# Performance work log

Measured on AMD Instinct MI355X. Metric: run time of the kernel, lower is better.

The kernel has to match this reference:

```python
import jax, jax.numpy as jnp
import numpy as np

B, S, H, NH, FF = 8, 512, 1024, 16, 4096
DK = H // NH


def _ln(x, g, b):
    m = x.mean(-1, keepdims=True)
    v = ((x - m) ** 2).mean(-1, keepdims=True)
    return (x - m) / jnp.sqrt(v + 1e-5) * g + b


def _fwd(x, predicate_pos, attn_bias, attention_mask, atom_graph, variable_graph,
         ln1_g, ln1_b, wq, bq, wk, bk, wv, bv, wo, bo,
         pq_w, pq_b, pk_w, pk_b, pv_w, pv_b, ln2_g, ln2_b, w1, b1, w2, b2):
    b_, s_, h_ = x.shape
    y = _ln(x, ln1_g, ln1_b)
    # ---- self attention (manual MHA with additive bias + mask) ----
    scale = DK ** -0.5
    q = (y @ wq + bq).reshape(b_, s_, NH, DK) * scale
    k = (y @ wk + bk).reshape(b_, s_, NH, DK)
    v = (y @ wv + bv).reshape(b_, s_, NH, DK)
    scores = jnp.einsum('bihd,bjhd->bhij', q, k)
    scores = scores + attn_bias[:, None, :, :] + attention_mask[:, None, :, :]
    att = jax.nn.softmax(scores, axis=-1)
    y_self = jnp.einsum('bhij,bjhd->bihd', att, v).reshape(b_, s_, h_) @ wo + bo
    # ---- path attention (single-head with graph biases) ----
    pscale = h_ ** -0.5
    pq = (y @ pq_w + pq_b) * pscale
    pk = y @ pk_w + pk_b
    pv = y @ pv_w + pv_b
    patt = jnp.einsum('bid,bjd->bij', pq, pk) + atom_graph + variable_graph
    patt = jax.nn.softmax(patt, axis=-1)
    xp = jnp.einsum('bij,bjd->bid', patt, pv)  # [B,S,H]
    # vectorized gather-mean over predicate positions (replaces per-sample loop)
    prev = jnp.concatenate([xp[:, :1], xp[:, :-1]], axis=1)   # xp[i-1]
    nxt = jnp.concatenate([xp[:, 1:], xp[:, -1:]], axis=1)    # xp[i+1]
    a0 = xp[:, 0:2].mean(axis=1, keepdims=True)               # i == 0
    a1 = xp[:, 0:3].mean(axis=1, keepdims=True)               # i == 1
    a2 = (xp + nxt) / 2.0                                     # pos[i-2] == 1
    a3 = (prev + xp + nxt) / 3.0                              # else
    i_arr = jnp.arange(s_)
    pos = (predicate_pos == 1)
    pos_m2 = jnp.pad(pos[:, :-2], ((0, 0), (2, 0)))           # pos[i-2], False for i<2
    atom = jnp.where(pos_m2[..., None], a2, a3)
    atom = jnp.where((i_arr == 1)[None, :, None], a1, atom)
    atom = jnp.where((i_arr == 0)[None, :, None], a0, atom)
    w = pos.astype(xp.dtype)
    path = (atom * w[..., None]).sum(1) / w.sum(1, keepdims=True)  # [B,H]
    y_path = jnp.broadcast_to(path[:, None, :], (b_, s_, h_))
    # ---- combine + residual + FFN ----
    x = x + (y_self + y_path) / 2.0
    y2 = _ln(x, ln2_g, ln2_b)
    hmid = jax.nn.gelu(y2 @ w1 + b1, approximate=False)
    return x + (hmid @ w2 + b2)


def setup_inputs() -> dict:
    key = jax.random.key(0)
    ks = jax.random.split(key, 16)
    def w(k, shape):
        return 0.02 * jax.random.normal(k, shape, dtype=jnp.float32)
    pp = jax.random.randint(ks[0], (B, S), 0, 2, dtype=jnp.int32)
    pp = pp.at[:, 2].set(1).at[:, -1].set(0)  # >=1 predicate; no predicate at last node
    return {
        'x': jax.random.normal(ks[1], (B, S, H), dtype=jnp.float32),
        'predicate_pos': pp,
        'variable_tags': jnp.zeros((B, S), dtype=jnp.int32),
        'attn_bias': 0.1 * jax.random.normal(ks[2], (B, S, S), dtype=jnp.float32),
        'attention_mask': jnp.zeros((B, S, S), dtype=jnp.float32),
        'atom_graph': 0.1 * jax.random.normal(ks[3], (B, S, S), dtype=jnp.float32),
        'variable_graph': 0.1 * jax.random.normal(ks[4], (B, S, S), dtype=jnp.float32),
        'ln1_g': jnp.ones((H,), jnp.float32), 'ln1_b': jnp.zeros((H,), jnp.float32),
        'wq': w(ks[5], (H, H)), 'bq': jnp.zeros((H,), jnp.float32),
        'wk': w(ks[6], (H, H)), 'bk': jnp.zeros((H,), jnp.float32),
        'wv': w(ks[7], (H, H)), 'bv': jnp.zeros((H,), jnp.float32),
        'wo': w(ks[8], (H, H)), 'bo': jnp.zeros((H,), jnp.float32),
        'pq_w': w(ks[9], (H, H)), 'pq_b': jnp.zeros((H,), jnp.float32),
        'pk_w': w(ks[10], (H, H)), 'pk_b': jnp.zeros((H,), jnp.float32),
        'pv_w': w(ks[11], (H, H)), 'pv_b': jnp.zeros((H,), jnp.float32),
        'ln2_g': jnp.ones((H,), jnp.float32), 'ln2_b': jnp.zeros((H,), jnp.float32),
        'w1': w(ks[12], (H, FF)), 'b1': jnp.zeros((FF,), jnp.float32),
        'w2': w(ks[13], (FF, H)), 'b2': jnp.zeros((H,), jnp.float32),
    }


def reference(x, predicate_pos, variable_tags, attn_bias, attention_mask, atom_graph, variable_graph,
              ln1_g, ln1_b, wq, bq, wk, bk, wv, bv, wo, bo,
              pq_w, pq_b, pk_w, pk_b, pv_w, pv_b, ln2_g, ln2_b, w1, b1, w2, b2):
    # variable_tags is unused in the original forward as well
    return _fwd(x, predicate_pos, attn_bias, attention_mask, atom_graph, variable_graph,
                ln1_g, ln1_b, wq, bq, wk, bk, wv, bv, wo, bo,
                pq_w, pq_b, pk_w, pk_b, pv_w, pv_b, ln2_g, ln2_b, w1, b1, w2, b2)
```

## Files before the change

kernel.cpp:

```cpp
#include <hip/hip_runtime.h>
#include <hip/hip_bf16.h>
#include <math.h>


typedef __bf16 bf16x8 __attribute__((ext_vector_type(8)));
typedef float f32x4 __attribute__((ext_vector_type(4)));

__device__ __forceinline__ void async_copy16(void* lds, const void* g) {
  __builtin_amdgcn_global_load_lds(
      (__attribute__((address_space(1))) void*)(void*)g,
      (__attribute__((address_space(3))) void*)lds, 16, 0, 0);
}

__global__ __launch_bounds__(256) void ln_rows_bf16(
    const float* __restrict__ X, const float* __restrict__ G,
    const float* __restrict__ Bt, __hip_bfloat16* __restrict__ O) {
  long row = blockIdx.x;
  int t = threadIdx.x;
  const float4 xv = ((const float4*)(X + row * 1024))[t];
  float s = xv.x + xv.y + xv.z + xv.w;
  float q = xv.x * xv.x + xv.y * xv.y + xv.z * xv.z + xv.w * xv.w;
#pragma unroll
  for (int o = 32; o; o >>= 1) {
    s += __shfl_xor(s, o);
    q += __shfl_xor(q, o);
  }
  __shared__ float rs[4], rq[4];
  int wid = t >> 6;
  if ((t & 63) == 0) { rs[wid] = s; rq[wid] = q; }
  __syncthreads();
  s = rs[0] + rs[1] + rs[2] + rs[3];
  q = rq[0] + rq[1] + rq[2] + rq[3];
  float mean = s * (1.f / 1024.f);
  float var = q * (1.f / 1024.f) - mean * mean;
  float rstd = rsqrtf(var + 1e-5f);
  const float4 gv = ((const float4*)G)[t];
  const float4 bv = ((const float4*)Bt)[t];
  __hip_bfloat16* o = O + row * 1024 + t * 4;
  o[0] = __float2bfloat16((xv.x - mean) * rstd * gv.x + bv.x);
  o[1] = __float2bfloat16((xv.y - mean) * rstd * gv.y + bv.y);
  o[2] = __float2bfloat16((xv.z - mean) * rstd * gv.z + bv.z);
  o[3] = __float2bfloat16((xv.w - mean) * rstd * gv.w + bv.w);
}

struct TC7 {
  const float* in[7];
  __hip_bfloat16* out[7];
  float scale[7];
};
__global__ __launch_bounds__(256) void tconv7(TC7 p) {
  __shared__ float t[32][33];
  int j = blockIdx.z;
  const float* in = p.in[j];
  __hip_bfloat16* out = p.out[j];
  float sc = p.scale[j];
  int c0 = blockIdx.x * 32, r0 = blockIdx.y * 32;
  int tid = threadIdx.x;
  int lr = tid >> 3, lc = (tid & 7) * 4;
  const float4 v = *(const float4*)&in[(long)(r0 + lr) * 1024 + c0 + lc];
  t[lr][lc] = v.x; t[lr][lc + 1] = v.y; t[lr][lc + 2] = v.z; t[lr][lc + 3] = v.w;
  __syncthreads();
  int oc = tid >> 3, orr = (tid & 7) * 4;
  __hip_bfloat16* o = &out[(long)(c0 + oc) * 1024 + r0 + orr];
  o[0] = __float2bfloat16(t[orr][oc] * sc);
  o[1] = __float2bfloat16(t[orr + 1][oc] * sc);
  o[2] = __float2bfloat16(t[orr + 2][oc] * sc);
  o[3] = __float2bfloat16(t[orr + 3][oc] * sc);
}

__global__ __launch_bounds__(256) void tconv_f32_bf16(
    const float* __restrict__ in, __hip_bfloat16* __restrict__ out, int R,
    int C) {
  __shared__ float t[32][33];
  int c0 = blockIdx.x * 32, r0 = blockIdx.y * 32;
  int tid = threadIdx.x;
  int lr = tid >> 3, lc = (tid & 7) * 4;
  const float4 v = *(const float4*)&in[(long)(r0 + lr) * C + c0 + lc];
  t[lr][lc] = v.x; t[lr][lc + 1] = v.y; t[lr][lc + 2] = v.z; t[lr][lc + 3] = v.w;
  __syncthreads();
  int oc = tid >> 3, orr = (tid & 7) * 4;
  __hip_bfloat16* o = &out[(long)(c0 + oc) * R + r0 + orr];
  o[0] = __float2bfloat16(t[orr][oc]);
  o[1] = __float2bfloat16(t[orr + 1][oc]);
  o[2] = __float2bfloat16(t[orr + 2][oc]);
  o[3] = __float2bfloat16(t[orr + 3][oc]);
}

__global__ __launch_bounds__(256) void tconv_bf16(
    const __hip_bfloat16* __restrict__ in, __hip_bfloat16* __restrict__ out,
    int R, int C, int ldin, long sIn) {
  __shared__ __hip_bfloat16 t[32][34];
  int bz = blockIdx.z;
  long ibase = (long)bz * sIn;
  long obase = (long)bz * R * C;
  int c0 = blockIdx.x * 32, r0 = blockIdx.y * 32;
  int tid = threadIdx.x;
  int lr = tid >> 3, lc = (tid & 7) * 4;
  const __hip_bfloat16* ip = &in[ibase + (long)(r0 + lr) * ldin + c0 + lc];
  t[lr][lc] = ip[0]; t[lr][lc + 1] = ip[1]; t[lr][lc + 2] = ip[2]; t[lr][lc + 3] = ip[3];
  __syncthreads();
  int oc = tid >> 3, orr = (tid & 7) * 4;
  __hip_bfloat16* o = &out[obase + (long)(c0 + oc) * R + r0 + orr];
  o[0] = t[orr][oc];
  o[1] = t[orr + 1][oc];
  o[2] = t[orr + 2][oc];
  o[3] = t[orr + 3][oc];
}

struct BC6 {
  const float* b[6];
  float scale[6];
};
__global__ __launch_bounds__(256) void bias_concat(BC6 p, float* __restrict__ o) {
  int idx = blockIdx.x * 256 + threadIdx.x;
  int j = idx >> 10, e = idx & 1023;
  o[idx] = p.b[j][e] * p.scale[j];
}

template <int BN>
__global__ __launch_bounds__(512, 2) void gemm256(
    const __hip_bfloat16* __restrict__ A, const __hip_bfloat16* __restrict__ Bt,
    const float* __restrict__ bias, void* __restrict__ C, int K, int lda,
    int ldb, int ldc, int act, int obf) {
  constexpr int NR = BN / 64;
  constexpr int ABYTES = 256 * 128;
  constexpr int BBYTES = BN * 128;
  constexpr int BUF = ABYTES + BBYTES;
  __shared__ char lds[2 * BUF];

  int nwg = gridDim.x * gridDim.y;
  int wg = blockIdx.y * gridDim.x + blockIdx.x;
  int cpx = nwg >> 3;
  int sw = (wg & 7) * cpx + (wg >> 3);
  int bx = sw % gridDim.x, by = sw / gridDim.x;
  const int m0 = by * 256, n0 = bx * BN;

  const int tid = threadIdx.x;
  const int lane = tid & 63, wid = tid >> 6;
  const int wm = wid >> 2, wn = wid & 3;
  const int ll = lane & 15, lh = lane >> 4;

  const char* Ag = (const char*)A;
  const char* Bg = (const char*)Bt;
  const int srow = tid >> 3;
  const int scb = (tid & 7) * 16;

  auto stage = [&](int t, int bsel) {
    char* base = lds + bsel * BUF;
    long kb = (long)t * 128;
#pragma unroll
    for (int l = 0; l < 4; ++l) {
      int row = l * 64 + srow;
      async_copy16(base + row * 128 + scb,
                   Ag + ((long)(m0 + row) * lda) * 2 + kb + scb);
    }
#pragma unroll
    for (int l = 0; l < BN / 64; ++l) {
      int row = l * 64 + srow;
      async_copy16(base + ABYTES + row * 128 + scb,
                   Bg + ((long)(n0 + row) * ldb) * 2 + kb + scb);
    }
  };

  f32x4 acc[8][NR];
#pragma unroll
  for (int m = 0; m < 8; ++m)
#pragma unroll
    for (int n = 0; n < NR; ++n) acc[m][n] = (f32x4){0.f, 0.f, 0.f, 0.f};

  const int nt = K >> 6;
  stage(0, 0);
  asm volatile("s_waitcnt vmcnt(0)" ::: "memory");
  __builtin_amdgcn_s_barrier();

  for (int t = 0; t < nt; ++t) {
    int bt = t & 1;
    if (t + 1 < nt) stage(t + 1, bt ^ 1);
    const char* Ab = lds + bt * BUF;
    const char* Bb = Ab + ABYTES;
#pragma unroll
    for (int ks = 0; ks < 2; ++ks) {
      bf16x8 af[8], bf[NR];
#pragma unroll
      for (int m = 0; m < 8; ++m)
        af[m] = *(const bf16x8*)(Ab + (wm * 128 + m * 16 + ll) * 128 +
                                 ks * 64 + lh * 16);
#pragma unroll
      for (int n = 0; n < NR; ++n)
        bf[n] = *(const bf16x8*)(Bb + (wn * (BN / 4) + n * 16 + ll) * 128 +
                                 ks * 64 + lh * 16);
      __builtin_amdgcn_s_setprio(1);
#pragma unroll
      for (int m = 0; m < 8; ++m)
#pragma unroll
        for (int n = 0; n < NR; ++n)
          acc[m][n] = __builtin_amdgcn_mfma_f32_16x16x32_bf16(af[m], bf[n],
                                                              acc[m][n], 0, 0, 0);
      __builtin_amdgcn_s_setprio(0);
    }
    asm volatile("s_waitcnt vmcnt(0)" ::: "memory");
    __builtin_amdgcn_s_barrier();
  }

#pragma unroll
  for (int m = 0; m < 8; ++m) {
    int row = m0 + wm * 128 + m * 16 + lh * 4;
#pragma unroll
    for (int n = 0; n < NR; ++n) {
      int col = n0 + wn * (BN / 4) + n * 16 + ll;
      float bs = bias ? bias[col] : 0.f;
#pragma unroll
      for (int r = 0; r < 4; ++r) {
        float v = acc[m][n][r] + bs;
        if (act) v = v * 0.5f * (1.f + erff(v * 0.70710678118f));
        long cidx = (long)(row + r) * ldc + col;
        if (obf)
          ((__hip_bfloat16*)C)[cidx] = __float2bfloat16(v);
        else
          ((float*)C)[cidx] = v;
      }
    }
  }
}

__global__ __launch_bounds__(256) void gemm_bf16_nt(
    const __hip_bfloat16* __restrict__ A, const __hip_bfloat16* __restrict__ Bt,
    const float* __restrict__ bias, const float* __restrict__ E1,
    const float* __restrict__ E2, void* __restrict__ C, int K, int lda,
    int ldb, int ldc, long sA, long sB, long sC, long sE, float alpha, int act,
    int obf) {
  __shared__ unsigned short AsU[128 * 32];
  __shared__ unsigned short BsU[128 * 32];
  const int tid = threadIdx.x;
  const int lane = tid & 63, wave = tid >> 6;
  const int wr = wave >> 1, wc = wave & 1;

  int nwg = gridDim.x * gridDim.y;
  int wg = blockIdx.y * gridDim.x + blockIdx.x;
  int bx = blockIdx.x, by = blockIdx.y;
  if ((nwg & 7) == 0) {
    int cpx = nwg >> 3;
    int sw = (wg & 7) * cpx + (wg >> 3);
    bx = sw % gridDim.x;
    by = sw / gridDim.x;
  }
  const int m0 = by * 128, n0 = bx * 128;
  const int bz = blockIdx.z;
  const char* Ab = (const char*)(A + (long)bz * sA);
  const char* Bb = (const char*)(Bt + (long)bz * sB);

  f32x4 acc[4][4];
#pragma unroll
  for (int m = 0; m < 4; ++m)
#pragma unroll
    for (int n = 0; n < 4; ++n) acc[m][n] = (f32x4){0.f, 0.f, 0.f, 0.f};

  const int srow = tid >> 2;
  const int scol = (tid & 3) * 16;
  const int wbase = (tid >> 6) * 1024;

  for (int k0 = 0; k0 < K; k0 += 32) {
#pragma unroll
    for (int i = 0; i < 2; ++i) {
      async_copy16((char*)AsU + i * 4096 + wbase,
                   Ab + ((long)(m0 + i * 64 + srow) * lda + k0) * 2 + scol);
      async_copy16((char*)BsU + i * 4096 + wbase,
                   Bb + ((long)(n0 + i * 64 + srow) * ldb + k0) * 2 + scol);
    }
    __syncthreads();

    const int koff = (lane >> 4) * 8;
    bf16x8 a[4], b[4];
#pragma unroll
    for (int m = 0; m < 4; ++m)
      a[m] = *(const bf16x8*)&AsU[(wr * 64 + m * 16 + (lane & 15)) * 32 + koff];
#pragma unroll
    for (int n = 0; n < 4; ++n)
      b[n] = *(const bf16x8*)&BsU[(wc * 64 + n * 16 + (lane & 15)) * 32 + koff];
#pragma unroll
    for (int m = 0; m < 4; ++m)
#pragma unroll
      for (int n = 0; n < 4; ++n)
        acc[m][n] = __builtin_amdgcn_mfma_f32_16x16x32_bf16(a[m], b[n],
                                                            acc[m][n], 0, 0, 0);
    __syncthreads();
  }

#pragma unroll
  for (int m = 0; m < 4; ++m) {
    int row = m0 + wr * 64 + m * 16 + (lane >> 4) * 4;
#pragma unroll
    for (int n = 0; n < 4; ++n) {
      int col = n0 + wc * 64 + n * 16 + (lane & 15);
      float bs = bias ? bias[col] : 0.f;
#pragma unroll
      for (int r = 0; r < 4; ++r) {
        float v = (acc[m][n][r] + bs) * alpha;
        long eidx = (long)bz * sE + (long)(row + r) * ldc + col;
        if (E1) v += E1[eidx];
        if (E2) v += E2[eidx];
        if (act) v = v * 0.5f * (1.f + erff(v * 0.70710678118f));
        long cidx = (long)bz * sC + (long)(row + r) * ldc + col;
        if (obf)
          ((__hip_bfloat16*)C)[cidx] = __float2bfloat16(v);
        else
          ((float*)C)[cidx] = v;
      }
    }
  }
}

__global__ __launch_bounds__(256) void attn_mfma(
    const __hip_bfloat16* __restrict__ Q, const __hip_bfloat16* __restrict__ K,
    const __hip_bfloat16* __restrict__ VT, const float* __restrict__ BiasP,
    const float* __restrict__ MaskP, __hip_bfloat16* __restrict__ O,
    int ldqk) {
  __shared__ __hip_bfloat16 P[32][520];
  __shared__ float red[2][32][4];
  const int it = blockIdx.x, h = blockIdx.y, b = blockIdx.z;
  const int i0 = it * 32;
  const int tid = threadIdx.x;
  const int lane = tid & 63, w = tid >> 6;
  const int lh = lane >> 4, ll = lane & 15;

  const long qkb = (long)b * 512 * ldqk + h * 64;

  bf16x8 a[2][2];
#pragma unroll
  for (int m = 0; m < 2; ++m)
#pragma unroll
    for (int ks = 0; ks < 2; ++ks)
      a[m][ks] = *(const bf16x8*)&Q[qkb + (long)(i0 + m * 16 + ll) * ldqk +
                                    ks * 32 + lh * 8];

  f32x4 acc[2][8];
#pragma unroll
  for (int m = 0; m < 2; ++m)
#pragma unroll
    for (int n = 0; n < 8; ++n) acc[m][n] = (f32x4){0.f, 0.f, 0.f, 0.f};

#pragma unroll
  for (int n = 0; n < 8; ++n) {
    const __hip_bfloat16* kp =
        &K[qkb + (long)(w * 128 + n * 16 + ll) * ldqk + lh * 8];
    bf16x8 b0 = *(const bf16x8*)&kp[0];
    bf16x8 b1 = *(const bf16x8*)&kp[32];
#pragma unroll
    for (int m = 0; m < 2; ++m) {
      acc[m][n] =
          __builtin_amdgcn_mfma_f32_16x16x32_bf16(a[m][0], b0, acc[m][n], 0, 0, 0);
      acc[m][n] =
          __builtin_amdgcn_mfma_f32_16x16x32_bf16(a[m][1], b1, acc[m][n], 0, 0, 0);
    }
  }

  const long bmo = ((long)b * 512 + i0) * 512 + w * 128;
#pragma unroll
  for (int m = 0; m < 2; ++m)
#pragma unroll
    for (int r = 0; r < 4; ++r) {
      int row = m * 16 + lh * 4 + r;
#pragma unroll
      for (int n = 0; n < 8; ++n) {
        long gi = bmo + (long)row * 512 + n * 16 + ll;
        acc[m][n][r] += BiasP[gi] + MaskP[gi];
      }
    }

  float rmax[2][4];
#pragma unroll
  for (int m = 0; m < 2; ++m)
#pragma unroll
    for (int r = 0; r < 4; ++r) {
      float v = acc[m][0][r];
#pragma unroll
      for (int n = 1; n < 8; ++n) v = fmaxf(v, acc[m][n][r]);
#pragma unroll
      for (int o = 1; o < 16; o <<= 1) v = fmaxf(v, __shfl_xor(v, o));
      rmax[m][r] = v;
    }
  if (ll == 0) {
#pragma unroll
    for (int m = 0; m < 2; ++m)
#pragma unroll
      for (int r = 0; r < 4; ++r) red[0][m * 16 + lh * 4 + r][w] = rmax[m][r];
  }
  __syncthreads();
#pragma unroll
  for (int m = 0; m < 2; ++m)
#pragma unroll
    for (int r = 0; r < 4; ++r) {
      const float* p = red[0][m * 16 + lh * 4 + r];
      rmax[m][r] = fmaxf(fmaxf(p[0], p[1]), fmaxf(p[2], p[3]));
    }
  float rsum[2][4];
#pragma unroll
  for (int m = 0; m < 2; ++m)
#pragma unroll
    for (int r = 0; r < 4; ++r) {
      float s = 0.f;
#pragma unroll
      for (int n = 0; n < 8; ++n) {
        float e = __expf(acc[m][n][r] - rmax[m][r]);
        acc[m][n][r] = e;
        s += e;
      }
#pragma unroll
      for (int o = 1; o < 16; o <<= 1) s += __shfl_xor(s, o);
      rsum[m][r] = s;
    }
  if (ll == 0) {
#pragma unroll
    for (int m = 0; m < 2; ++m)
#pragma unroll
      for (int r = 0; r < 4; ++r) red[1][m * 16 + lh * 4 + r][w] = rsum[m][r];
  }
  __syncthreads();
#pragma unroll
  for (int m = 0; m < 2; ++m)
#pragma unroll
    for (int r = 0; r < 4; ++r) {
      const float* p = red[1][m * 16 + lh * 4 + r];
      float inv = 1.f / (p[0] + p[1] + p[2] + p[3]);
      int row = m * 16 + lh * 4 + r;
#pragma unroll
      for (int n = 0; n < 8; ++n)
        P[row][w * 128 + n * 16 + ll] = __float2bfloat16(acc[m][n][r] * inv);
    }
  __syncthreads();

  const long vtb = ((long)b * 1024 + h * 64) * 512;
  const long ob = (long)b * 512 * 1024 + h * 64;
  const int mw = (w >> 1) * 16, nw = (w & 1) * 32;
  f32x4 oacc[2];
  oacc[0] = (f32x4){0.f, 0.f, 0.f, 0.f};
  oacc[1] = (f32x4){0.f, 0.f, 0.f, 0.f};
#pragma unroll
  for (int ks = 0; ks < 16; ++ks) {
    int k0 = ks * 32;
    bf16x8 pa = *(const bf16x8*)&P[mw + ll][k0 + lh * 8];
#pragma unroll
    for (int nf = 0; nf < 2; ++nf) {
      bf16x8 vb = *(const bf16x8*)&VT[vtb + (long)(nw + nf * 16 + ll) * 512 +
                                      k0 + lh * 8];
      oacc[nf] =
          __builtin_amdgcn_mfma_f32_16x16x32_bf16(pa, vb, oacc[nf], 0, 0, 0);
    }
  }
#pragma unroll
  for (int nf = 0; nf < 2; ++nf)
#pragma unroll
    for (int r = 0; r < 4; ++r)
      O[ob + (long)(i0 + mw + lh * 4 + r) * 1024 + nw + nf * 16 + ll] =
          __float2bfloat16(oacc[nf][r]);
}

__global__ __launch_bounds__(256) void softmax_rows(
    const float* __restrict__ P, __hip_bfloat16* __restrict__ Ob) {
  const float* row = P + (long)blockIdx.x * 512;
  __hip_bfloat16* orow = Ob + (long)blockIdx.x * 512;
  int t = threadIdx.x;
  float v0 = row[t], v1 = row[t + 256];
  float m = fmaxf(v0, v1);
#pragma unroll
  for (int o = 32; o; o >>= 1) m = fmaxf(m, __shfl_xor(m, o));
  __shared__ float red[8];
  int wid = t >> 6, lane = t & 63;
  if (!lane) red[wid] = m;
  __syncthreads();
  m = fmaxf(fmaxf(red[0], red[1]), fmaxf(red[2], red[3]));
  float e0 = __expf(v0 - m), e1 = __expf(v1 - m);
  float s = e0 + e1;
#pragma unroll
  for (int o = 32; o; o >>= 1) s += __shfl_xor(s, o);
  if (!lane) red[4 + wid] = s;
  __syncthreads();
  s = red[4] + red[5] + red[6] + red[7];
  float inv = 1.f / s;
  orow[t] = __float2bfloat16(e0 * inv);
  orow[t + 256] = __float2bfloat16(e1 * inv);
}

__global__ __launch_bounds__(256) void path_partial(
    const float* __restrict__ xp, const int* __restrict__ pp,
    float* __restrict__ PP, float* __restrict__ WS) {
  int b = blockIdx.x, hc = blockIdx.y, ic = blockIdx.z;
  int h = hc * 256 + threadIdx.x;
  const int* ppb = pp + b * 512;
  const float* xb = xp + (long)b * 512 * 1024;
  int iA = ic * 64, iB = iA + 64;
  float acc = 0.f;
  for (int i = iA; i < iB; ++i) {
    if (ppb[i] != 1) continue;
    float cur = xb[(long)i * 1024 + h];
    float a;
    if (i == 0) {
      a = 0.5f * (cur + xb[1024 + h]);
    } else if (i == 1) {
      a = (xb[h] + cur + xb[2 * 1024 + h]) * (1.f / 3.f);
    } else {
      int inx = (i + 1 < 512) ? i + 1 : 511;
      float nx = xb[(long)inx * 1024 + h];
      if (ppb[i - 2] == 1) {
        a = 0.5f * (cur + nx);
      } else {
        a = (xb[(long)(i - 1) * 1024 + h] + cur + nx) * (1.f / 3.f);
      }
    }
    acc += a;
  }
  PP[((long)b * 8 + ic) * 1024 + h] = acc;
  if (hc == 0 && threadIdx.x == 0) {
    float c = 0.f;
    for (int i = iA; i < iB; ++i) c += (ppb[i] == 1) ? 1.f : 0.f;
    WS[b * 8 + ic] = c;
  }
}

__global__ __launch_bounds__(256) void path_finalize(
    const float* __restrict__ PP, const float* __restrict__ WS,
    float* __restrict__ PATH) {
  int b = blockIdx.x;
  int h = blockIdx.y * 256 + threadIdx.x;
  float s = 0.f, w = 0.f;
#pragma unroll
  for (int ic = 0; ic < 8; ++ic) {
    s += PP[((long)b * 8 + ic) * 1024 + h];
    w += WS[b * 8 + ic];
  }
  PATH[b * 1024 + h] = s / w;
}

__global__ __launch_bounds__(256) void combine_ln2(
    const float* __restrict__ X, const float* __restrict__ YS,
    const float* __restrict__ PT, const float* __restrict__ G,
    const float* __restrict__ Bt, float* __restrict__ X2,
    __hip_bfloat16* __restrict__ Y2b) {
  long row = blockIdx.x;
  int b = (int)(row >> 9);
  int t = threadIdx.x;
  const float4 xv = ((const float4*)(X + row * 1024))[t];
  const float4 sv = ((const float4*)(YS + row * 1024))[t];
  const float4 pv = *(const float4*)(PT + b * 1024 + t * 4);
  float4 v;
  v.x = xv.x + 0.5f * (sv.x + pv.x);
  v.y = xv.y + 0.5f * (sv.y + pv.y);
  v.z = xv.z + 0.5f * (sv.z + pv.z);
  v.w = xv.w + 0.5f * (sv.w + pv.w);
  ((float4*)(X2 + row * 1024))[t] = v;

  float s = v.x + v.y + v.z + v.w;
  float q = v.x * v.x + v.y * v.y + v.z * v.z + v.w * v.w;
#pragma unroll
  for (int o = 32; o; o >>= 1) {
    s += __shfl_xor(s, o);
    q += __shfl_xor(q, o);
  }
  __shared__ float rs[4], rq[4];
  int wid = t >> 6;
  if ((t & 63) == 0) { rs[wid] = s; rq[wid] = q; }
  __syncthreads();
  s = rs[0] + rs[1] + rs[2] + rs[3];
  q = rq[0] + rq[1] + rq[2] + rq[3];
  float mean = s * (1.f / 1024.f);
  float var = q * (1.f / 1024.f) - mean * mean;
  float rstd = rsqrtf(var + 1e-5f);
  const float4 gv = ((const float4*)G)[t];
  const float4 bv = ((const float4*)Bt)[t];
  __hip_bfloat16* o = Y2b + row * 1024 + t * 4;
  o[0] = __float2bfloat16((v.x - mean) * rstd * gv.x + bv.x);
  o[1] = __float2bfloat16((v.y - mean) * rstd * gv.y + bv.y);
  o[2] = __float2bfloat16((v.z - mean) * rstd * gv.z + bv.z);
  o[3] = __float2bfloat16((v.w - mean) * rstd * gv.w + bv.w);
}

extern "C" void kernel_launch(void* const* d_in, const int* in_sizes, int n_in,
                              void* d_out, int out_size, void* d_ws,
                              size_t ws_size, hipStream_t stream) {
  const float* x = (const float*)d_in[0];
  const int* pp = (const int*)d_in[1];
  const float* abias = (const float*)d_in[3];
  const float* amask = (const float*)d_in[4];
  const float* agraph = (const float*)d_in[5];
  const float* vgraph = (const float*)d_in[6];
  const float* ln1g = (const float*)d_in[7];
  const float* ln1b = (const float*)d_in[8];
  const float* wq = (const float*)d_in[9];
  const float* bq = (const float*)d_in[10];
  const float* wk = (const float*)d_in[11];
  const float* bk = (const float*)d_in[12];
  const float* wv = (const float*)d_in[13];
  const float* bv = (const float*)d_in[14];
  const float* wo = (const float*)d_in[15];
  const float* bo = (const float*)d_in[16];
  const float* pqw = (const float*)d_in[17];
  const float* pqb = (const float*)d_in[18];
  const float* pkw = (const float*)d_in[19];
  const float* pkb = (const float*)d_in[20];
  const float* pvw = (const float*)d_in[21];
  const float* pvb = (const float*)d_in[22];
  const float* ln2g = (const float*)d_in[23];
  const float* ln2b = (const float*)d_in[24];
  const float* w1 = (const float*)d_in[25];
  const float* b1 = (const float*)d_in[26];
  const float* w2 = (const float*)d_in[27];
  const float* b2 = (const float*)d_in[28];

  char* wsb = (char*)d_ws;
  auto Ybf = (__hip_bfloat16*)(wsb);
  auto QKV = (__hip_bfloat16*)(wsb + (8l << 20));
  auto VTb = (__hip_bfloat16*)(wsb + (56l << 20));
  auto PVT = (__hip_bfloat16*)(wsb + (64l << 20));
  auto ATTb = (__hip_bfloat16*)(wsb + (72l << 20));
  auto PATTb = (__hip_bfloat16*)(wsb + (88l << 20));
  auto PATTf = (float*)(wsb + (92l << 20));
  auto XP = (float*)(wsb + (92l << 20));
  auto WALL = (__hip_bfloat16*)(wsb + (108l << 20));
  auto WOT = (__hip_bfloat16*)(wsb + (120l << 20));
  auto W1T = (__hip_bfloat16*)(wsb + (122l << 20));
  auto bias6 = (float*)(wsb + (130l << 20));
  auto PPart = (float*)(wsb + (131l << 20));
  auto WSp = (float*)(wsb + (132l << 20));
  auto PATH = (float*)(wsb + (133l << 20));
  auto YSELF = (float*)(wsb + (8l << 20));
  auto X2 = (float*)(wsb + (24l << 20));
  auto HMID = (__hip_bfloat16*)(wsb + (40l << 20));
  auto W2T = ATTb;
  __hip_bfloat16* Y2b = Ybf;
  float* OUT = (float*)d_out;

  const float qscale = 0.125f;
  const float pscale = 0.03125f;
  const long S2 = 512l * 512;
  const long SQ = 512l * 6144;

  __hip_bfloat16* Qp = QKV;
  __hip_bfloat16* Kp = QKV + 1024;
  __hip_bfloat16* Vp = QKV + 2048;
  __hip_bfloat16* PQp = QKV + 3072;
  __hip_bfloat16* PKp = QKV + 4096;
  __hip_bfloat16* PVp = QKV + 5120;

  TC7 tp;
  tp.in[0] = wq;  tp.out[0] = WALL;                 tp.scale[0] = qscale;
  tp.in[1] = wk;  tp.out[1] = WALL + 1024 * 1024;   tp.scale[1] = 1.f;
  tp.in[2] = wv;  tp.out[2] = WALL + 2048 * 1024;   tp.scale[2] = 1.f;
  tp.in[3] = pqw; tp.out[3] = WALL + 3072 * 1024;   tp.scale[3] = pscale;
  tp.in[4] = pkw; tp.out[4] = WALL + 4096 * 1024;   tp.scale[4] = 1.f;
  tp.in[5] = pvw; tp.out[5] = WALL + 5120 * 1024;   tp.scale[5] = 1.f;
  tp.in[6] = wo;  tp.out[6] = WOT;                  tp.scale[6] = 1.f;
  tconv7<<<dim3(32, 32, 7), 256, 0, stream>>>(tp);
  tconv_f32_bf16<<<dim3(128, 32), 256, 0, stream>>>(w1, W1T, 1024, 4096);

  BC6 bp;
  bp.b[0] = bq;  bp.scale[0] = qscale;
  bp.b[1] = bk;  bp.scale[1] = 1.f;
  bp.b[2] = bv;  bp.scale[2] = 1.f;
  bp.b[3] = pqb; bp.scale[3] = pscale;
  bp.b[4] = pkb; bp.scale[4] = 1.f;
  bp.b[5] = pvb; bp.scale[5] = 1.f;
  bias_concat<<<24, 256, 0, stream>>>(bp, bias6);

  ln_rows_bf16<<<4096, 256, 0, stream>>>(x, ln1g, ln1b, Ybf);

  gemm256<128><<<dim3(48, 16), 512, 0, stream>>>(
      Ybf, WALL, bias6, QKV, 1024, 1024, 1024, 6144, 0, 1);

  tconv_bf16<<<dim3(32, 16, 8), 256, 0, stream>>>(Vp, VTb, 512, 1024, 6144, SQ);
  tconv_bf16<<<dim3(32, 16, 8), 256, 0, stream>>>(PVp, PVT, 512, 1024, 6144, SQ);

  gemm_bf16_nt<<<dim3(4, 4, 8), 256, 0, stream>>>(
      PQp, PKp, nullptr, agraph, vgraph, PATTf, 1024, 6144, 6144, 512, SQ, SQ,
      S2, S2, 1.f, 0, 0);
  softmax_rows<<<4096, 256, 0, stream>>>(PATTf, PATTb);

  attn_mfma<<<dim3(16, 16, 8), 256, 0, stream>>>(Qp, Kp, VTb, abias, amask,
                                                 ATTb, 6144);

  gemm_bf16_nt<<<dim3(8, 4, 8), 256, 0, stream>>>(
      PATTb, PVT, nullptr, nullptr, nullptr, XP, 512, 512, 512, 1024, S2,
      512l * 1024, 512l * 1024, 0, 1.f, 0, 0);

  path_partial<<<dim3(8, 4, 8), 256, 0, stream>>>(XP, pp, PPart, WSp);
  path_finalize<<<dim3(8, 4), 256, 0, stream>>>(PPart, WSp, PATH);

  gemm_bf16_nt<<<dim3(8, 32, 1), 256, 0, stream>>>(
      ATTb, WOT, bo, nullptr, nullptr, YSELF, 1024, 1024, 1024, 1024, 0, 0, 0,
      0, 1.f, 0, 0);

  tconv_f32_bf16<<<dim3(32, 128), 256, 0, stream>>>(w2, W2T, 4096, 1024);

  combine_ln2<<<4096, 256, 0, stream>>>(x, YSELF, PATH, ln2g, ln2b, X2, Y2b);

  gemm256<256><<<dim3(16, 16), 512, 0, stream>>>(
      Y2b, W1T, b1, HMID, 1024, 1024, 1024, 4096, 1, 1);

  gemm_bf16_nt<<<dim3(8, 32, 1), 256, 0, stream>>>(
      HMID, W2T, b2, X2, nullptr, OUT, 4096, 4096, 4096, 1024, 0, 0, 0, 0, 1.f,
      0, 0);
}
```

Baseline: 531.1 us.

## Run FFN2 GEMM as split-K over the large-tile kernel with a reduction pass

The second FFN GEMM (K=4096, output 4096x1024) moves from the 128x128 generic GEMM to the 256-tile gemm256 kernel with a 4-way split-K over blockIdx.z, writing fp32 partials. A new reduction kernel sums the four partials, adds the bias and the residual X2, and writes the output. The aim is a faster MFMA kernel with enough workgroups (8x16x4) to fill the GPU. The cost is 64MB of extra partial-sum traffic and one more kernel launch.

```diff
diff --git a/kernel.cpp b/kernel.cpp
--- a/kernel.cpp
+++ b/kernel.cpp
@@ -121,7 +121,7 @@
 __global__ __launch_bounds__(512, 2) void gemm256(
     const __hip_bfloat16* __restrict__ A, const __hip_bfloat16* __restrict__ Bt,
     const float* __restrict__ bias, void* __restrict__ C, int K, int lda,
-    int ldb, int ldc, int act, int obf) {
+    int ldb, int ldc, int act, int obf, long sC) {
   constexpr int NR = BN / 64;
   constexpr int ABYTES = 256 * 128;
   constexpr int BBYTES = BN * 128;
@@ -134,6 +134,8 @@
   int sw = (wg & 7) * cpx + (wg >> 3);
   int bx = sw % gridDim.x, by = sw / gridDim.x;
   const int m0 = by * 256, n0 = bx * BN;
+  const int z = blockIdx.z;
+  const long kbase = (long)z * K * 2;
 
   const int tid = threadIdx.x;
   const int lane = tid & 63, wid = tid >> 6;
@@ -147,7 +149,7 @@
 
   auto stage = [&](int t, int bsel) {
     char* base = lds + bsel * BUF;
-    long kb = (long)t * 128;
+    long kb = kbase + (long)t * 128;
 #pragma unroll
     for (int l = 0; l < 4; ++l) {
       int row = l * 64 + srow;
@@ -213,7 +215,7 @@
       for (int r = 0; r < 4; ++r) {
         float v = acc[m][n][r] + bs;
         if (act) v = v * 0.5f * (1.f + erff(v * 0.70710678118f));
-        long cidx = (long)(row + r) * ldc + col;
+        long cidx = (long)z * sC + (long)(row + r) * ldc + col;
         if (obf)
           ((__hip_bfloat16*)C)[cidx] = __float2bfloat16(v);
         else
@@ -221,6 +223,25 @@
       }
     }
   }
+}
+
+__global__ __launch_bounds__(256) void ffn2_reduce(
+    const float* __restrict__ P, const float* __restrict__ X2,
+    const float* __restrict__ b2, float* __restrict__ OUT) {
+  int i = blockIdx.x * 256 + threadIdx.x;
+  const long SP = 4194304;
+  float4 a = ((const float4*)P)[i];
+  float4 b = ((const float4*)(P + SP))[i];
+  float4 c = ((const float4*)(P + 2 * SP))[i];
+  float4 d = ((const float4*)(P + 3 * SP))[i];
+  float4 xr = ((const float4*)X2)[i];
+  const float4 bb = *(const float4*)(b2 + ((i & 255) * 4));
+  float4 o;
+  o.x = a.x + b.x + c.x + d.x + xr.x + bb.x;
+  o.y = a.y + b.y + c.y + d.y + xr.y + bb.y;
+  o.z = a.z + b.z + c.z + d.z + xr.z + bb.z;
+  o.w = a.w + b.w + c.w + d.w + xr.w + bb.w;
+  ((float4*)OUT)[i] = o;
 }
 
 __global__ __launch_bounds__(256) void gemm_bf16_nt(
@@ -626,6 +647,7 @@
   auto X2 = (float*)(wsb + (24l << 20));
   auto HMID = (__hip_bfloat16*)(wsb + (40l << 20));
   auto W2T = ATTb;
+  auto PART = (float*)(wsb + (92l << 20));
   __hip_bfloat16* Y2b = Ybf;
   float* OUT = (float*)d_out;
 
@@ -663,8 +685,8 @@
 
   ln_rows_bf16<<<4096, 256, 0, stream>>>(x, ln1g, ln1b, Ybf);
 
-  gemm256<128><<<dim3(48, 16), 512, 0, stream>>>(
-      Ybf, WALL, bias6, QKV, 1024, 1024, 1024, 6144, 0, 1);
+  gemm256<128><<<dim3(48, 16, 1), 512, 0, stream>>>(
+      Ybf, WALL, bias6, QKV, 1024, 1024, 1024, 6144, 0, 1, 0);
 
   tconv_bf16<<<dim3(32, 16, 8), 256, 0, stream>>>(Vp, VTb, 512, 1024, 6144, SQ);
   tconv_bf16<<<dim3(32, 16, 8), 256, 0, stream>>>(PVp, PVT, 512, 1024, 6144, SQ);
@@ -692,10 +714,11 @@
 
   combine_ln2<<<4096, 256, 0, stream>>>(x, YSELF, PATH, ln2g, ln2b, X2, Y2b);
 
-  gemm256<256><<<dim3(16, 16), 512, 0, stream>>>(
-      Y2b, W1T, b1, HMID, 1024, 1024, 1024, 4096, 1, 1);
-
-  gemm_bf16_nt<<<dim3(8, 32, 1), 256, 0, stream>>>(
-      HMID, W2T, b2, X2, nullptr, OUT, 4096, 4096, 4096, 1024, 0, 0, 0, 0, 1.f,
-      0, 0);
-}
+  gemm256<256><<<dim3(16, 16, 1), 512, 0, stream>>>(
+      Y2b, W1T, b1, HMID, 1024, 1024, 1024, 4096, 1, 1, 0);
+
+  gemm256<128><<<dim3(8, 16, 4), 512, 0, stream>>>(
+      HMID, W2T, nullptr, PART, 1024, 4096, 4096, 1024, 0, 0, 4194304);
+
+  ffn2_reduce<<<4096, 256, 0, stream>>>(PART, X2, b2, OUT);
+}
```

Result: no change. 530.1 us (-0.2%).
